# Optimization experiments

Measured on AMD Instinct MI355X. Metric: run time of the kernel, lower is better.

## Reference

```python
import jax, jax.numpy as jnp
import numpy as np

BEV_RANGE = 32.0   # meters; traj xy normalized to [-1,1] by this half-range
NUM_HEADS = 8
EGO_FUT_TS = 8
EPS = 1e-5


def _ln(x, g, b):
    m = x.mean(-1, keepdims=True)
    v = ((x - m) ** 2).mean(-1, keepdims=True)
    return (x - m) / jnp.sqrt(v + EPS) * g + b


def _mha(q, k, v, wq, bq, wk, bk, wv, bv, wo, bo):
    B, Lq, D = q.shape
    Lk = k.shape[1]
    dh = D // NUM_HEADS
    qh = (q @ wq + bq).reshape(B, Lq, NUM_HEADS, dh).transpose(0, 2, 1, 3)
    kh = (k @ wk + bk).reshape(B, Lk, NUM_HEADS, dh).transpose(0, 2, 1, 3)
    vh = (v @ wv + bv).reshape(B, Lk, NUM_HEADS, dh).transpose(0, 2, 1, 3)
    a = jax.nn.softmax(jnp.einsum('bhqd,bhkd->bhqk', qh, kh) * (1.0 / float(np.sqrt(dh))), axis=-1)
    o = jnp.einsum('bhqk,bhkd->bhqd', a, vh).transpose(0, 2, 1, 3).reshape(B, Lq, D)
    return o @ wo + bo


def _grid_sample(value, grid):
    # value (B,C,H,W); grid (B,M,P,2) xy in [-1,1]; bilinear, zeros padding, align_corners=False
    B, C, H, W = value.shape
    x = (grid[..., 0] + 1.0) * (W * 0.5) - 0.5
    y = (grid[..., 1] + 1.0) * (H * 0.5) - 0.5
    x0 = jnp.floor(x)
    y0 = jnp.floor(y)
    bidx = jnp.arange(B)[:, None, None]

    def corner(xi, yi, w):
        valid = (xi >= 0) & (xi <= W - 1) & (yi >= 0) & (yi <= H - 1)
        xc = jnp.clip(xi, 0, W - 1).astype(jnp.int32)
        yc = jnp.clip(yi, 0, H - 1).astype(jnp.int32)
        v = value[bidx, :, yc, xc]  # advanced idx -> (B,M,P,C)
        return v * (w * valid)[..., None]

    return (corner(x0, y0, (x0 + 1 - x) * (y0 + 1 - y))
            + corner(x0 + 1, y0, (x - x0) * (y0 + 1 - y))
            + corner(x0, y0 + 1, (x0 + 1 - x) * (y - y0))
            + corner(x0 + 1, y0 + 1, (x - x0) * (y - y0)))


def _mish(x):
    return x * jnp.tanh(jax.nn.softplus(x))


def _forward(traj_feature, noisy_traj_points, bev_feature, agents_query, ego_query,
             time_embed, status_encoding,
             bev_value_w, bev_value_b, bev_attn_w, bev_attn_b, bev_out_w, bev_out_b,
             aq_wq, aq_bq, aq_wk, aq_bk, aq_wv, aq_bv, aq_wo, aq_bo,
             eq_wq, eq_bq, eq_wk, eq_bk, eq_wv, eq_bv, eq_wo, eq_bo,
             ffn_w1, ffn_b1, ffn_w2, ffn_b2,
             n1_g, n1_b, n2_g, n2_b, n3_g, n3_b,
             mod_w, mod_b,
             cls_w1, cls_b1, cls_ln1_g, cls_ln1_b, cls_w2, cls_b2, cls_ln2_g, cls_ln2_b, cls_w3, cls_b3,
             reg_w1, reg_b1, reg_w2, reg_b2, reg_w3, reg_b3):
    B, M, D = traj_feature.shape
    # --- GridSampleCrossBEVAttention ---
    value = jnp.einsum('bchw,cd->bdhw', bev_feature, bev_value_w) + bev_value_b[None, :, None, None]
    grid = noisy_traj_points / BEV_RANGE                    # (B,M,P,2) in [-1,1]
    sampled = _grid_sample(value, grid)                     # (B,M,P,D)
    pt_w = jax.nn.softmax(traj_feature @ bev_attn_w + bev_attn_b, axis=-1)  # (B,M,P)
    bev_out = jnp.einsum('bmpd,bmp->bmd', sampled, pt_w) @ bev_out_w + bev_out_b
    traj = traj_feature + bev_out
    # --- cross-agent attention + norm1 ---
    traj = _ln(traj + _mha(traj, agents_query, agents_query,
                           aq_wq, aq_bq, aq_wk, aq_bk, aq_wv, aq_bv, aq_wo, aq_bo), n1_g, n1_b)
    # --- cross-ego attention + norm2 ---
    traj = _ln(traj + _mha(traj, ego_query, ego_query,
                           eq_wq, eq_bq, eq_wk, eq_bk, eq_wv, eq_bv, eq_wo, eq_bo), n2_g, n2_b)
    # --- FFN + norm3 (note: no residual, matches source) ---
    traj = _ln(jax.nn.relu(traj @ ffn_w1 + ffn_b1) @ ffn_w2 + ffn_b2, n3_g, n3_b)
    # --- FiLM time modulation ---
    ss = _mish(time_embed) @ mod_w + mod_b                  # (B,1,2D)
    scale, shift = jnp.split(ss, 2, axis=-1)
    traj = traj * (1.0 + scale) + shift
    # --- task decoder: cls branch (linear_relu_ln x2 + Linear->1) ---
    h = _ln(jax.nn.relu(traj @ cls_w1 + cls_b1), cls_ln1_g, cls_ln1_b)
    h = _ln(jax.nn.relu(h @ cls_w2 + cls_b2), cls_ln2_g, cls_ln2_b)
    plan_cls = (h @ cls_w3 + cls_b3)[..., 0]                # (B,M)
    # --- task decoder: reg branch ---
    r = jax.nn.relu(traj @ reg_w1 + reg_b1)
    r = jax.nn.relu(r @ reg_w2 + reg_b2)
    r = (r @ reg_w3 + reg_b3).reshape(B, M, EGO_FUT_TS, 3)
    xy = r[..., :2] + noisy_traj_points
    heading = jnp.tanh(r[..., 2:3]) * np.pi
    poses_reg = jnp.concatenate([xy, heading], axis=-1)     # (B,M,T,3)
    return poses_reg, plan_cls


def setup_inputs() -> dict:
    key = jax.random.key(0)
    ks = iter(jax.random.split(key, 80))
    rn = lambda *s: jax.random.normal(next(ks), s, dtype=jnp.float32)
    w = lambda *s: rn(*s) * 0.05
    B, M, P, D, A, FF = 32, 20, 8, 256, 32, 1024
    inp = dict(
        traj_feature=rn(B, M, D),
        noisy_traj_points=rn(B, M, P, 2) * 8.0,
        bev_feature=rn(B, 256, 128, 128),
        agents_query=rn(B, A, D),
        ego_query=rn(B, 1, D),
        time_embed=rn(B, 1, D),
        status_encoding=rn(B, 1, D),
        bev_value_w=w(256, D), bev_value_b=jnp.zeros(D),
        bev_attn_w=w(D, P), bev_attn_b=jnp.zeros(P),
        bev_out_w=w(D, D), bev_out_b=jnp.zeros(D),
        aq_wq=w(D, D), aq_bq=jnp.zeros(D), aq_wk=w(D, D), aq_bk=jnp.zeros(D),
        aq_wv=w(D, D), aq_bv=jnp.zeros(D), aq_wo=w(D, D), aq_bo=jnp.zeros(D),
        eq_wq=w(D, D), eq_bq=jnp.zeros(D), eq_wk=w(D, D), eq_bk=jnp.zeros(D),
        eq_wv=w(D, D), eq_bv=jnp.zeros(D), eq_wo=w(D, D), eq_bo=jnp.zeros(D),
        ffn_w1=w(D, FF), ffn_b1=jnp.zeros(FF), ffn_w2=w(FF, D), ffn_b2=jnp.zeros(D),
        n1_g=jnp.ones(D), n1_b=jnp.zeros(D), n2_g=jnp.ones(D), n2_b=jnp.zeros(D),
        n3_g=jnp.ones(D), n3_b=jnp.zeros(D),
        mod_w=w(D, 2 * D), mod_b=jnp.zeros(2 * D),
        cls_w1=w(D, D), cls_b1=jnp.zeros(D), cls_ln1_g=jnp.ones(D), cls_ln1_b=jnp.zeros(D),
        cls_w2=w(D, D), cls_b2=jnp.zeros(D), cls_ln2_g=jnp.ones(D), cls_ln2_b=jnp.zeros(D),
        cls_w3=w(D, 1), cls_b3=jnp.full((1,), float(-np.log((1 - 0.01) / 0.01))),
        reg_w1=w(D, D), reg_b1=jnp.zeros(D), reg_w2=w(D, D), reg_b2=jnp.zeros(D),
        reg_w3=w(D, EGO_FUT_TS * 3), reg_b3=jnp.zeros(EGO_FUT_TS * 3),
        bev_spatial_shape=jnp.array([128, 128], dtype=jnp.int32),
    )
    return inp


def reference(traj_feature, noisy_traj_points, bev_feature, agents_query, ego_query,
              time_embed, status_encoding,
              bev_value_w, bev_value_b, bev_attn_w, bev_attn_b, bev_out_w, bev_out_b,
              aq_wq, aq_bq, aq_wk, aq_bk, aq_wv, aq_bv, aq_wo, aq_bo,
              eq_wq, eq_bq, eq_wk, eq_bk, eq_wv, eq_bv, eq_wo, eq_bo,
              ffn_w1, ffn_b1, ffn_w2, ffn_b2,
              n1_g, n1_b, n2_g, n2_b, n3_g, n3_b,
              mod_w, mod_b,
              cls_w1, cls_b1, cls_ln1_g, cls_ln1_b, cls_w2, cls_b2, cls_ln2_g, cls_ln2_b, cls_w3, cls_b3,
              reg_w1, reg_b1, reg_w2, reg_b2, reg_w3, reg_b3,
              bev_spatial_shape):
    # bev_spatial_shape is implied by bev_feature's static shape under jit
    return _forward(traj_feature, noisy_traj_points, bev_feature, agents_query, ego_query,
                    time_embed, status_encoding,
                    bev_value_w, bev_value_b, bev_attn_w, bev_attn_b, bev_out_w, bev_out_b,
                    aq_wq, aq_bq, aq_wk, aq_bk, aq_wv, aq_bv, aq_wo, aq_bo,
                    eq_wq, eq_bq, eq_wk, eq_bk, eq_wv, eq_bv, eq_wo, eq_bo,
                    ffn_w1, ffn_b1, ffn_w2, ffn_b2,
                    n1_g, n1_b, n2_g, n2_b, n3_g, n3_b,
                    mod_w, mod_b,
                    cls_w1, cls_b1, cls_ln1_g, cls_ln1_b, cls_w2, cls_b2, cls_ln2_g, cls_ln2_b, cls_w3, cls_b3,
                    reg_w1, reg_b1, reg_w2, reg_b2, reg_w3, reg_b3)
```

## Files before the change

kernel.cpp:

```cpp
#include <hip/hip_runtime.h>
#include <math.h>

constexpr int NB = 32;
constexpr int NM = 20;
constexpr int NP = 8;
constexpr int ND = 256;
constexpr int NA = 32;
constexpr int NFF = 1024;
constexpr int NH = 128, NW = 128;
constexpr int HW = NH * NW;

constexpr int PK_BVW = 0;
constexpr int PK_BOW = 65536;
constexpr int PK_WQ  = 131072;
constexpr int PK_WO  = 196608;
constexpr int PK_CW1 = 262144;
constexpr int PK_CW2 = 327680;
constexpr int PK_RW1 = 393216;
constexpr int PK_RW2 = 458752;
constexpr int PK_WK  = 524288;
constexpr int PK_WV  = 589824;
constexpr int PK_FW1 = 655360;
constexpr int PK_FW2 = 917504;
constexpr int PK_TOTAL = 1179648;

constexpr int WS_GW   = 0;
constexpr int WS_WSUM = 163840;
constexpr int WS_K1   = 164480;
constexpr int WS_V1   = 426624;
constexpr int WS_U    = 688768;
constexpr int WS_SS   = 696960;
constexpr int WS_PACK = 720896;

__device__ __forceinline__ void dec2(unsigned u, float& f0, float& f1) {
    union { unsigned x; float f; } a, b;
    a.x = u << 16;
    b.x = u & 0xffff0000u;
    f0 = a.f; f1 = b.f;
}

__device__ __forceinline__ float fma4(float4 a, uint2 w, float acc) {
    float w0, w1, w2, w3;
    dec2(w.x, w0, w1);
    dec2(w.y, w2, w3);
    acc += a.x * w0;
    acc += a.y * w1;
    acc += a.z * w2;
    acc += a.w * w3;
    return acc;
}

__device__ __forceinline__ float gemm256(const uint2* __restrict__ wp, const float* __restrict__ sa,
                                         int tid, float acc) {
    const float4* a4 = (const float4*)sa;
    #pragma unroll 8
    for (int c4 = 0; c4 < 64; ++c4) {
        float4 a = a4[c4];
        uint2 w = wp[(c4 << 8) + tid];
        acc = fma4(a, w, acc);
    }
    return acc;
}

struct PackArgs {
    const float* src[12];
    int log2N[12];
    int elems[12];
    int dstoff[12];
};

__global__ void pack_kernel(PackArgs pa, unsigned short* __restrict__ dst) {
    int e = blockIdx.x * 256 + threadIdx.x;
    int seg = 0;
    while (seg < 12 && e >= pa.elems[seg]) { e -= pa.elems[seg]; seg++; }
    if (seg >= 12) return;
    int lg = pa.log2N[seg];
    int N = 1 << lg;
    int c = e >> lg;
    int n = e & (N - 1);
    float v = pa.src[seg][e];
    union { float f; unsigned u; } uu; uu.f = v;
    unsigned x = uu.u;
    unsigned r = (x + 0x7fff + ((x >> 16) & 1)) >> 16;
    int idx = (((c >> 2) << lg) + n) * 4 + (c & 3);
    dst[pa.dstoff[seg] + idx] = (unsigned short)r;
}

__device__ __forceinline__ float blk_sum(float v, float* s_red) {
    for (int off = 32; off > 0; off >>= 1) v += __shfl_down(v, off, 64);
    int tid = threadIdx.x;
    __syncthreads();
    if ((tid & 63) == 0) s_red[tid >> 6] = v;
    __syncthreads();
    return s_red[0] + s_red[1] + s_red[2] + s_red[3];
}

__device__ __forceinline__ float blk_ln(float x, const float* g, const float* bb, float* s_red) {
    int tid = threadIdx.x;
    float mean = blk_sum(x, s_red) * (1.0f / 256.0f);
    float xm = x - mean;
    float var = blk_sum(xm * xm, s_red) * (1.0f / 256.0f);
    return xm / sqrtf(var + 1e-5f) * g[tid] + bb[tid];
}

__global__ void gather_kernel(const float* __restrict__ traj, const float* __restrict__ noisy,
                              const float* __restrict__ bev, const float* __restrict__ attn_w,
                              const float* __restrict__ attn_b,
                              float* __restrict__ gw, float* __restrict__ wsumw) {
    int blk = blockIdx.x;
    int b = blk / NM, tid = threadIdx.x;
    __shared__ float s_traj[ND];
    __shared__ float s_ptw[NP];
    __shared__ float s_w[32];
    __shared__ int s_idx[32];

    s_traj[tid] = traj[(size_t)blk * ND + tid];
    __syncthreads();
    if (tid < NP) {
        float acc = attn_b[tid];
        for (int c = 0; c < ND; c++) acc += s_traj[c] * attn_w[c * NP + tid];
        s_ptw[tid] = acc;
    }
    __syncthreads();
    if (tid == 0) {
        float mx = s_ptw[0];
        for (int p = 1; p < NP; p++) mx = fmaxf(mx, s_ptw[p]);
        float e[NP], sum = 0.f;
        for (int p = 0; p < NP; p++) { e[p] = expf(s_ptw[p] - mx); sum += e[p]; }
        for (int p = 0; p < NP; p++) s_ptw[p] = e[p] / sum;
    }
    __syncthreads();
    if (tid < 32) {
        int p = tid >> 2, corner = tid & 3;
        float gx = noisy[((size_t)blk * NP + p) * 2 + 0] * (1.0f / 32.0f);
        float gy = noisy[((size_t)blk * NP + p) * 2 + 1] * (1.0f / 32.0f);
        float x = (gx + 1.0f) * (NW * 0.5f) - 0.5f;
        float y = (gy + 1.0f) * (NH * 0.5f) - 0.5f;
        float x0 = floorf(x), y0 = floorf(y);
        int dx = corner & 1, dy = corner >> 1;
        float wx = dx ? (x - x0) : (x0 + 1.0f - x);
        float wy = dy ? (y - y0) : (y0 + 1.0f - y);
        float xi = x0 + (float)dx, yi = y0 + (float)dy;
        bool valid = (xi >= 0.f) && (xi <= (float)(NW - 1)) && (yi >= 0.f) && (yi <= (float)(NH - 1));
        int xc = (int)fminf(fmaxf(xi, 0.f), (float)(NW - 1));
        int yc = (int)fminf(fmaxf(yi, 0.f), (float)(NH - 1));
        s_w[tid] = wx * wy * (valid ? 1.f : 0.f) * s_ptw[p];
        s_idx[tid] = yc * NW + xc;
    }
    __syncthreads();
    if (tid == 0) {
        float s = 0.f;
        for (int j = 0; j < 32; j++) s += s_w[j];
        wsumw[blk] = s;
    }
    const float* base = bev + (size_t)b * ND * HW + (size_t)tid * HW;
    float acc0 = 0.f, acc1 = 0.f;
    #pragma unroll
    for (int j = 0; j < 32; j += 2) {
        acc0 += s_w[j]     * base[s_idx[j]];
        acc1 += s_w[j + 1] * base[s_idx[j + 1]];
    }
    gw[(size_t)blk * ND + tid] = acc0 + acc1;
}

__global__ void kv_kernel(const float* __restrict__ agents,
                          const uint2* __restrict__ wkp, const float* __restrict__ bk,
                          const uint2* __restrict__ wvp, const float* __restrict__ bv,
                          float* __restrict__ K1, float* __restrict__ V1) {
    int blk = blockIdx.x, tid = threadIdx.x;
    int a0 = blk * 2;
    __shared__ __align__(16) float s0[ND], s1[ND];
    s0[tid] = agents[(size_t)a0 * ND + tid];
    s1[tid] = agents[(size_t)(a0 + 1) * ND + tid];
    __syncthreads();
    float k0 = bk[tid], k1 = k0, v0 = bv[tid], v1 = v0;
    const float4* p0 = (const float4*)s0;
    const float4* p1 = (const float4*)s1;
    #pragma unroll 8
    for (int c4 = 0; c4 < 64; ++c4) {
        float4 a0f = p0[c4], a1f = p1[c4];
        uint2 wk = wkp[(c4 << 8) + tid];
        uint2 wv = wvp[(c4 << 8) + tid];
        k0 = fma4(a0f, wk, k0); k1 = fma4(a1f, wk, k1);
        v0 = fma4(a0f, wv, v0); v1 = fma4(a1f, wv, v1);
    }
    K1[(size_t)a0 * ND + tid] = k0;
    K1[(size_t)(a0 + 1) * ND + tid] = k1;
    V1[(size_t)a0 * ND + tid] = v0;
    V1[(size_t)(a0 + 1) * ND + tid] = v1;
}

__global__ void perb_kernel(const float* __restrict__ ego,
                            const float* __restrict__ eq_wv, const float* __restrict__ eq_bv,
                            const float* __restrict__ eq_wo, const float* __restrict__ eq_bo,
                            const float* __restrict__ time_embed,
                            const float* __restrict__ mod_w, const float* __restrict__ mod_b,
                            float* __restrict__ u, float* __restrict__ ss) {
    int b = blockIdx.x, tid = threadIdx.x;
    __shared__ float s_a[ND], s_b[ND];
    s_a[tid] = ego[(size_t)b * ND + tid];
    __syncthreads();
    float v = eq_bv[tid];
    for (int c = 0; c < ND; c++) v += s_a[c] * eq_wv[c * ND + tid];
    s_b[tid] = v;
    __syncthreads();
    float o = eq_bo[tid];
    for (int c = 0; c < ND; c++) o += s_b[c] * eq_wo[c * ND + tid];
    u[(size_t)b * ND + tid] = o;

    float te = time_embed[(size_t)b * ND + tid];
    float sp = log1pf(expf(te));
    float me = te * tanhf(sp);
    __syncthreads();
    s_a[tid] = me;
    __syncthreads();
    for (int jj = 0; jj < 2; jj++) {
        int j = tid + jj * ND;
        float acc = mod_b[j];
        for (int c = 0; c < ND; c++) acc += s_a[c] * mod_w[(size_t)c * 2 * ND + j];
        ss[(size_t)b * 2 * ND + j] = acc;
    }
}

struct MegaW {
    const float *traj, *noisy;
    const float *bvb, *bob, *bq, *bo;
    const float *n1g, *n1b, *n2g, *n2b;
    const float *fb1, *fb2, *n3g, *n3b;
    const float *cb1, *cl1g, *cl1b, *cb2, *cl2g, *cl2b, *cw3, *cb3;
    const float *rb1, *rb2, *rw3, *rb3;
};

__global__ void mega_kernel(const float* __restrict__ gw, const float* __restrict__ wsumw,
                            const float* __restrict__ K1, const float* __restrict__ V1,
                            const float* __restrict__ u, const float* __restrict__ ss,
                            const uint2* __restrict__ bvwp, const uint2* __restrict__ bowp,
                            const uint2* __restrict__ wqp, const uint2* __restrict__ wop,
                            const uint2* __restrict__ fw1p, const uint2* __restrict__ fw2p,
                            const uint2* __restrict__ cw1p, const uint2* __restrict__ cw2p,
                            const uint2* __restrict__ rw1p, const uint2* __restrict__ rw2p,
                            MegaW W, float* __restrict__ out) {
    int blk = blockIdx.x;
    int b = blk / NM, tid = threadIdx.x;
    __shared__ __align__(16) float s_a[ND];
    __shared__ __align__(16) float s_b[ND];
    __shared__ __align__(16) float s_h[NFF];
    __shared__ __align__(16) float s_sc[ND];
    __shared__ float s_red[4];

    s_sc[tid] = gw[(size_t)blk * ND + tid];
    float wsw = wsumw[blk];
    __syncthreads();
    float acc = gemm256(bvwp, s_sc, tid, W.bvb[tid] * wsw);
    __syncthreads();
    s_b[tid] = acc;
    __syncthreads();
    acc = gemm256(bowp, s_b, tid, W.bob[tid] + W.traj[(size_t)blk * ND + tid]);
    s_a[tid] = acc;
    __syncthreads();
    acc = gemm256(wqp, s_a, tid, W.bq[tid]);
    __syncthreads();
    s_b[tid] = acc;
    __syncthreads();
    int h = tid >> 5, kk = tid & 31;
    {
        const float* Krow = K1 + ((size_t)(b * NA + kk)) * ND + h * 32;
        float sc = 0.f;
        for (int j = 0; j < 32; j++) sc += s_b[h * 32 + j] * Krow[j];
        s_sc[tid] = sc * 0.17677669529663687f;
    }
    __syncthreads();
    {
        float mx = -1e30f;
        for (int j = 0; j < 32; j++) mx = fmaxf(mx, s_sc[h * 32 + j]);
        float den = 0.f;
        for (int j = 0; j < 32; j++) den += expf(s_sc[h * 32 + j] - mx);
        float p = expf(s_sc[tid] - mx) / den;
        __syncthreads();
        s_sc[tid] = p;
        __syncthreads();
    }
    {
        const float* Vb = V1 + (size_t)b * NA * ND;
        float o = 0.f;
        for (int k = 0; k < 32; k++) o += s_sc[h * 32 + k] * Vb[(size_t)k * ND + tid];
        __syncthreads();
        s_b[tid] = o;
        __syncthreads();
    }
    acc = gemm256(wop, s_b, tid, W.bo[tid] + s_a[tid]);
    float t1 = blk_ln(acc, W.n1g, W.n1b, s_red);
    float t2 = blk_ln(t1 + u[(size_t)b * ND + tid], W.n2g, W.n2b, s_red);
    __syncthreads();
    s_a[tid] = t2;
    __syncthreads();
    {
        float f0 = W.fb1[tid], f1 = W.fb1[tid + 256], f2 = W.fb1[tid + 512], f3 = W.fb1[tid + 768];
        const float4* a4 = (const float4*)s_a;
        #pragma unroll 4
        for (int c4 = 0; c4 < 64; ++c4) {
            float4 a = a4[c4];
            f0 = fma4(a, fw1p[(c4 << 10) + tid], f0);
            f1 = fma4(a, fw1p[(c4 << 10) + 256 + tid], f1);
            f2 = fma4(a, fw1p[(c4 << 10) + 512 + tid], f2);
            f3 = fma4(a, fw1p[(c4 << 10) + 768 + tid], f3);
        }
        s_h[tid] = fmaxf(f0, 0.f);
        s_h[tid + 256] = fmaxf(f1, 0.f);
        s_h[tid + 512] = fmaxf(f2, 0.f);
        s_h[tid + 768] = fmaxf(f3, 0.f);
    }
    __syncthreads();
    {
        acc = W.fb2[tid];
        const float4* h4 = (const float4*)s_h;
        #pragma unroll 8
        for (int c4 = 0; c4 < 256; ++c4) {
            acc = fma4(h4[c4], fw2p[(c4 << 8) + tid], acc);
        }
    }
    float t3 = blk_ln(acc, W.n3g, W.n3b, s_red);
    float sc1 = ss[(size_t)b * 2 * ND + tid];
    float sh1 = ss[(size_t)b * 2 * ND + ND + tid];
    float tt = t3 * (1.f + sc1) + sh1;
    __syncthreads();
    s_a[tid] = tt;
    __syncthreads();
    acc = gemm256(cw1p, s_a, tid, W.cb1[tid]);
    float h1 = blk_ln(fmaxf(acc, 0.f), W.cl1g, W.cl1b, s_red);
    __syncthreads();
    s_b[tid] = h1;
    __syncthreads();
    acc = gemm256(cw2p, s_b, tid, W.cb2[tid]);
    float h2 = blk_ln(fmaxf(acc, 0.f), W.cl2g, W.cl2b, s_red);
    float pc = blk_sum(h2 * W.cw3[tid], s_red);
    if (tid == 0) out[(size_t)NB * NM * NP * 3 + blk] = pc + W.cb3[0];
    acc = gemm256(rw1p, s_a, tid, W.rb1[tid]);
    __syncthreads();
    s_b[tid] = fmaxf(acc, 0.f);
    __syncthreads();
    acc = gemm256(rw2p, s_b, tid, W.rb2[tid]);
    __syncthreads();
    s_b[tid] = fmaxf(acc, 0.f);
    __syncthreads();
    if (tid < 24) {
        float r3 = W.rb3[tid];
        for (int c = 0; c < ND; c++) r3 += s_b[c] * W.rw3[c * 24 + tid];
        int ts = tid / 3, k2 = tid % 3;
        float val;
        if (k2 < 2) val = r3 + W.noisy[((size_t)blk * NP + ts) * 2 + k2];
        else        val = tanhf(r3) * 3.14159265358979323846f;
        out[((size_t)blk * NP + ts) * 3 + k2] = val;
    }
}

extern "C" void kernel_launch(void* const* d_in, const int* in_sizes, int n_in,
                              void* d_out, int out_size, void* d_ws, size_t ws_size,
                              hipStream_t stream) {
    const float* traj   = (const float*)d_in[0];
    const float* noisy  = (const float*)d_in[1];
    const float* bev    = (const float*)d_in[2];
    const float* agents = (const float*)d_in[3];
    const float* ego    = (const float*)d_in[4];
    const float* temb   = (const float*)d_in[5];
    const float* bvw = (const float*)d_in[7];
    const float* bvb = (const float*)d_in[8];
    const float* baw = (const float*)d_in[9];
    const float* bab = (const float*)d_in[10];
    const float* bow = (const float*)d_in[11];
    const float* bob = (const float*)d_in[12];
    const float* aq_wq = (const float*)d_in[13];
    const float* aq_bq = (const float*)d_in[14];
    const float* aq_wk = (const float*)d_in[15];
    const float* aq_bk = (const float*)d_in[16];
    const float* aq_wv = (const float*)d_in[17];
    const float* aq_bv = (const float*)d_in[18];
    const float* aq_wo = (const float*)d_in[19];
    const float* aq_bo = (const float*)d_in[20];
    const float* eq_wv = (const float*)d_in[25];
    const float* eq_bv = (const float*)d_in[26];
    const float* eq_wo = (const float*)d_in[27];
    const float* eq_bo = (const float*)d_in[28];
    const float* fw1 = (const float*)d_in[29];
    const float* fb1 = (const float*)d_in[30];
    const float* fw2 = (const float*)d_in[31];
    const float* fb2 = (const float*)d_in[32];
    const float* n1g = (const float*)d_in[33];
    const float* n1b = (const float*)d_in[34];
    const float* n2g = (const float*)d_in[35];
    const float* n2b = (const float*)d_in[36];
    const float* n3g = (const float*)d_in[37];
    const float* n3b = (const float*)d_in[38];
    const float* modw = (const float*)d_in[39];
    const float* modb = (const float*)d_in[40];
    const float* cw1 = (const float*)d_in[41];
    const float* cb1 = (const float*)d_in[42];
    const float* cl1g = (const float*)d_in[43];
    const float* cl1b = (const float*)d_in[44];
    const float* cw2 = (const float*)d_in[45];
    const float* cb2 = (const float*)d_in[46];
    const float* cl2g = (const float*)d_in[47];
    const float* cl2b = (const float*)d_in[48];
    const float* cw3 = (const float*)d_in[49];
    const float* cb3 = (const float*)d_in[50];
    const float* rw1 = (const float*)d_in[51];
    const float* rb1 = (const float*)d_in[52];
    const float* rw2 = (const float*)d_in[53];
    const float* rb2 = (const float*)d_in[54];
    const float* rw3 = (const float*)d_in[55];
    const float* rb3 = (const float*)d_in[56];

    float* ws = (float*)d_ws;
    float* gw    = ws + WS_GW;
    float* wsumw = ws + WS_WSUM;
    float* K1    = ws + WS_K1;
    float* V1    = ws + WS_V1;
    float* u     = ws + WS_U;
    float* ssb   = ws + WS_SS;
    unsigned short* pk = (unsigned short*)(ws + WS_PACK);

    PackArgs pa;
    const float* srcs[12] = {bvw, bow, aq_wq, aq_wo, cw1, cw2, rw1, rw2, aq_wk, aq_wv, fw1, fw2};
    int lg[12]   = {8, 8, 8, 8, 8, 8, 8, 8, 8, 8, 10, 8};
    int el[12]   = {65536, 65536, 65536, 65536, 65536, 65536, 65536, 65536, 65536, 65536, 262144, 262144};
    int off[12]  = {PK_BVW, PK_BOW, PK_WQ, PK_WO, PK_CW1, PK_CW2, PK_RW1, PK_RW2, PK_WK, PK_WV, PK_FW1, PK_FW2};
    for (int i = 0; i < 12; i++) { pa.src[i] = srcs[i]; pa.log2N[i] = lg[i]; pa.elems[i] = el[i]; pa.dstoff[i] = off[i]; }
    pack_kernel<<<dim3(PK_TOTAL / 256), dim3(256), 0, stream>>>(pa, pk);

    gather_kernel<<<dim3(NB * NM), dim3(256), 0, stream>>>(traj, noisy, bev, baw, bab, gw, wsumw);
    kv_kernel<<<dim3(NB * NA / 2), dim3(256), 0, stream>>>(agents,
        (const uint2*)(pk + PK_WK), aq_bk, (const uint2*)(pk + PK_WV), aq_bv, K1, V1);
    perb_kernel<<<dim3(NB), dim3(256), 0, stream>>>(ego, eq_wv, eq_bv, eq_wo, eq_bo, temb, modw, modb, u, ssb);

    MegaW W;
    W.traj = traj; W.noisy = noisy;
    W.bvb = bvb; W.bob = bob; W.bq = aq_bq; W.bo = aq_bo;
    W.n1g = n1g; W.n1b = n1b; W.n2g = n2g; W.n2b = n2b;
    W.fb1 = fb1; W.fb2 = fb2; W.n3g = n3g; W.n3b = n3b;
    W.cb1 = cb1; W.cl1g = cl1g; W.cl1b = cl1b;
    W.cb2 = cb2; W.cl2g = cl2g; W.cl2b = cl2b; W.cw3 = cw3; W.cb3 = cb3;
    W.rb1 = rb1; W.rb2 = rb2; W.rw3 = rw3; W.rb3 = rb3;

    mega_kernel<<<dim3(NB * NM), dim3(256), 0, stream>>>(gw, wsumw, K1, V1, u, ssb,
        (const uint2*)(pk + PK_BVW), (const uint2*)(pk + PK_BOW),
        (const uint2*)(pk + PK_WQ),  (const uint2*)(pk + PK_WO),
        (const uint2*)(pk + PK_FW1), (const uint2*)(pk + PK_FW2),
        (const uint2*)(pk + PK_CW1), (const uint2*)(pk + PK_CW2),
        (const uint2*)(pk + PK_RW1), (const uint2*)(pk + PK_RW2),
        W, (float*)d_out);
}
```

Baseline: 890.9 us.

## Fuse prologue kernels into one launch and process two tokens per mega block

Merges the pack, gather, K/V projection and per-batch kernels into a single prologue kernel, dispatching on block index. The K/V projection now reads fp32 weights directly, four agents per block, so those weights no longer need packing first. The mega kernel runs 512-thread blocks that each handle two tokens, with reductions split per half-block. The aim is to cut launch and dependency overhead and reuse weight loads across two tokens, at the cost of more shared memory per block and occupancy limits set through launch bounds.

```diff
diff --git a/kernel.cpp b/kernel.cpp
--- a/kernel.cpp
+++ b/kernel.cpp
@@ -18,11 +18,9 @@
 constexpr int PK_CW2 = 327680;
 constexpr int PK_RW1 = 393216;
 constexpr int PK_RW2 = 458752;
-constexpr int PK_WK  = 524288;
-constexpr int PK_WV  = 589824;
 constexpr int PK_FW1 = 655360;
 constexpr int PK_FW2 = 917504;
-constexpr int PK_TOTAL = 1179648;
+constexpr int PK_ELEMS = 1048576;
 
 constexpr int WS_GW   = 0;
 constexpr int WS_WSUM = 163840;
@@ -51,175 +49,181 @@
 }
 
 __device__ __forceinline__ float gemm256(const uint2* __restrict__ wp, const float* __restrict__ sa,
-                                         int tid, float acc) {
+                                         int t, float acc) {
     const float4* a4 = (const float4*)sa;
     #pragma unroll 8
     for (int c4 = 0; c4 < 64; ++c4) {
         float4 a = a4[c4];
-        uint2 w = wp[(c4 << 8) + tid];
+        uint2 w = wp[(c4 << 8) + t];
         acc = fma4(a, w, acc);
     }
     return acc;
 }
 
+constexpr int GB_GATHER = NB * NM;
+constexpr int GB_KV     = NB * NA / 4;
+constexpr int GB_PERB   = NB;
+constexpr int GB_PACK   = PK_ELEMS / 256;
+constexpr int PRO_GRID  = GB_GATHER + GB_KV + GB_PERB + GB_PACK;
+
 struct PackArgs {
-    const float* src[12];
-    int log2N[12];
-    int elems[12];
-    int dstoff[12];
+    const float* src[10];
+    int log2N[10];
+    int elems[10];
+    int dstoff[10];
 };
 
-__global__ void pack_kernel(PackArgs pa, unsigned short* __restrict__ dst) {
-    int e = blockIdx.x * 256 + threadIdx.x;
-    int seg = 0;
-    while (seg < 12 && e >= pa.elems[seg]) { e -= pa.elems[seg]; seg++; }
-    if (seg >= 12) return;
-    int lg = pa.log2N[seg];
-    int N = 1 << lg;
-    int c = e >> lg;
-    int n = e & (N - 1);
-    float v = pa.src[seg][e];
-    union { float f; unsigned u; } uu; uu.f = v;
-    unsigned x = uu.u;
-    unsigned r = (x + 0x7fff + ((x >> 16) & 1)) >> 16;
-    int idx = (((c >> 2) << lg) + n) * 4 + (c & 3);
-    dst[pa.dstoff[seg] + idx] = (unsigned short)r;
-}
-
-__device__ __forceinline__ float blk_sum(float v, float* s_red) {
-    for (int off = 32; off > 0; off >>= 1) v += __shfl_down(v, off, 64);
-    int tid = threadIdx.x;
-    __syncthreads();
-    if ((tid & 63) == 0) s_red[tid >> 6] = v;
-    __syncthreads();
-    return s_red[0] + s_red[1] + s_red[2] + s_red[3];
-}
-
-__device__ __forceinline__ float blk_ln(float x, const float* g, const float* bb, float* s_red) {
-    int tid = threadIdx.x;
-    float mean = blk_sum(x, s_red) * (1.0f / 256.0f);
-    float xm = x - mean;
-    float var = blk_sum(xm * xm, s_red) * (1.0f / 256.0f);
-    return xm / sqrtf(var + 1e-5f) * g[tid] + bb[tid];
-}
-
-__global__ void gather_kernel(const float* __restrict__ traj, const float* __restrict__ noisy,
-                              const float* __restrict__ bev, const float* __restrict__ attn_w,
-                              const float* __restrict__ attn_b,
-                              float* __restrict__ gw, float* __restrict__ wsumw) {
-    int blk = blockIdx.x;
-    int b = blk / NM, tid = threadIdx.x;
-    __shared__ float s_traj[ND];
+struct ProArgs {
+    const float *traj, *noisy, *bev, *attn_w, *attn_b;
+    const float *agents, *wk, *bk, *wv, *bv;
+    const float *ego, *eq_wv, *eq_bv, *eq_wo, *eq_bo;
+    const float *temb, *modw, *modb;
+    float *gw, *wsum, *K1, *V1, *u, *ss;
+    unsigned short* pk;
+};
+
+__global__ void prologue_kernel(ProArgs A, PackArgs pa) {
+    int blk = blockIdx.x, tid = threadIdx.x;
+    __shared__ __align__(16) float sm0[ND];
+    __shared__ __align__(16) float sm1[ND];
+    __shared__ __align__(16) float sm2[ND];
+    __shared__ __align__(16) float sm3[ND];
     __shared__ float s_ptw[NP];
     __shared__ float s_w[32];
     __shared__ int s_idx[32];
 
-    s_traj[tid] = traj[(size_t)blk * ND + tid];
-    __syncthreads();
-    if (tid < NP) {
-        float acc = attn_b[tid];
-        for (int c = 0; c < ND; c++) acc += s_traj[c] * attn_w[c * NP + tid];
-        s_ptw[tid] = acc;
-    }
-    __syncthreads();
-    if (tid == 0) {
-        float mx = s_ptw[0];
-        for (int p = 1; p < NP; p++) mx = fmaxf(mx, s_ptw[p]);
-        float e[NP], sum = 0.f;
-        for (int p = 0; p < NP; p++) { e[p] = expf(s_ptw[p] - mx); sum += e[p]; }
-        for (int p = 0; p < NP; p++) s_ptw[p] = e[p] / sum;
-    }
-    __syncthreads();
-    if (tid < 32) {
-        int p = tid >> 2, corner = tid & 3;
-        float gx = noisy[((size_t)blk * NP + p) * 2 + 0] * (1.0f / 32.0f);
-        float gy = noisy[((size_t)blk * NP + p) * 2 + 1] * (1.0f / 32.0f);
-        float x = (gx + 1.0f) * (NW * 0.5f) - 0.5f;
-        float y = (gy + 1.0f) * (NH * 0.5f) - 0.5f;
-        float x0 = floorf(x), y0 = floorf(y);
-        int dx = corner & 1, dy = corner >> 1;
-        float wx = dx ? (x - x0) : (x0 + 1.0f - x);
-        float wy = dy ? (y - y0) : (y0 + 1.0f - y);
-        float xi = x0 + (float)dx, yi = y0 + (float)dy;
-        bool valid = (xi >= 0.f) && (xi <= (float)(NW - 1)) && (yi >= 0.f) && (yi <= (float)(NH - 1));
-        int xc = (int)fminf(fmaxf(xi, 0.f), (float)(NW - 1));
-        int yc = (int)fminf(fmaxf(yi, 0.f), (float)(NH - 1));
-        s_w[tid] = wx * wy * (valid ? 1.f : 0.f) * s_ptw[p];
-        s_idx[tid] = yc * NW + xc;
-    }
-    __syncthreads();
-    if (tid == 0) {
-        float s = 0.f;
-        for (int j = 0; j < 32; j++) s += s_w[j];
-        wsumw[blk] = s;
-    }
-    const float* base = bev + (size_t)b * ND * HW + (size_t)tid * HW;
-    float acc0 = 0.f, acc1 = 0.f;
-    #pragma unroll
-    for (int j = 0; j < 32; j += 2) {
-        acc0 += s_w[j]     * base[s_idx[j]];
-        acc1 += s_w[j + 1] * base[s_idx[j + 1]];
-    }
-    gw[(size_t)blk * ND + tid] = acc0 + acc1;
-}
-
-__global__ void kv_kernel(const float* __restrict__ agents,
-                          const uint2* __restrict__ wkp, const float* __restrict__ bk,
-                          const uint2* __restrict__ wvp, const float* __restrict__ bv,
-                          float* __restrict__ K1, float* __restrict__ V1) {
-    int blk = blockIdx.x, tid = threadIdx.x;
-    int a0 = blk * 2;
-    __shared__ __align__(16) float s0[ND], s1[ND];
-    s0[tid] = agents[(size_t)a0 * ND + tid];
-    s1[tid] = agents[(size_t)(a0 + 1) * ND + tid];
-    __syncthreads();
-    float k0 = bk[tid], k1 = k0, v0 = bv[tid], v1 = v0;
-    const float4* p0 = (const float4*)s0;
-    const float4* p1 = (const float4*)s1;
-    #pragma unroll 8
-    for (int c4 = 0; c4 < 64; ++c4) {
-        float4 a0f = p0[c4], a1f = p1[c4];
-        uint2 wk = wkp[(c4 << 8) + tid];
-        uint2 wv = wvp[(c4 << 8) + tid];
-        k0 = fma4(a0f, wk, k0); k1 = fma4(a1f, wk, k1);
-        v0 = fma4(a0f, wv, v0); v1 = fma4(a1f, wv, v1);
-    }
-    K1[(size_t)a0 * ND + tid] = k0;
-    K1[(size_t)(a0 + 1) * ND + tid] = k1;
-    V1[(size_t)a0 * ND + tid] = v0;
-    V1[(size_t)(a0 + 1) * ND + tid] = v1;
-}
-
-__global__ void perb_kernel(const float* __restrict__ ego,
-                            const float* __restrict__ eq_wv, const float* __restrict__ eq_bv,
-                            const float* __restrict__ eq_wo, const float* __restrict__ eq_bo,
-                            const float* __restrict__ time_embed,
-                            const float* __restrict__ mod_w, const float* __restrict__ mod_b,
-                            float* __restrict__ u, float* __restrict__ ss) {
-    int b = blockIdx.x, tid = threadIdx.x;
-    __shared__ float s_a[ND], s_b[ND];
-    s_a[tid] = ego[(size_t)b * ND + tid];
-    __syncthreads();
-    float v = eq_bv[tid];
-    for (int c = 0; c < ND; c++) v += s_a[c] * eq_wv[c * ND + tid];
-    s_b[tid] = v;
-    __syncthreads();
-    float o = eq_bo[tid];
-    for (int c = 0; c < ND; c++) o += s_b[c] * eq_wo[c * ND + tid];
-    u[(size_t)b * ND + tid] = o;
-
-    float te = time_embed[(size_t)b * ND + tid];
-    float sp = log1pf(expf(te));
-    float me = te * tanhf(sp);
-    __syncthreads();
-    s_a[tid] = me;
-    __syncthreads();
-    for (int jj = 0; jj < 2; jj++) {
-        int j = tid + jj * ND;
-        float acc = mod_b[j];
-        for (int c = 0; c < ND; c++) acc += s_a[c] * mod_w[(size_t)c * 2 * ND + j];
-        ss[(size_t)b * 2 * ND + j] = acc;
-    }
+    if (blk < GB_GATHER) {
+        int b = blk / NM;
+        sm0[tid] = A.traj[(size_t)blk * ND + tid];
+        __syncthreads();
+        if (tid < NP) {
+            float acc = A.attn_b[tid];
+            for (int c = 0; c < ND; c++) acc += sm0[c] * A.attn_w[c * NP + tid];
+            s_ptw[tid] = acc;
+        }
+        __syncthreads();
+        if (tid == 0) {
+            float mx = s_ptw[0];
+            for (int p = 1; p < NP; p++) mx = fmaxf(mx, s_ptw[p]);
+            float e[NP], sum = 0.f;
+            for (int p = 0; p < NP; p++) { e[p] = expf(s_ptw[p] - mx); sum += e[p]; }
+            for (int p = 0; p < NP; p++) s_ptw[p] = e[p] / sum;
+        }
+        __syncthreads();
+        if (tid < 32) {
+            int p = tid >> 2, corner = tid & 3;
+            float gx = A.noisy[((size_t)blk * NP + p) * 2 + 0] * (1.0f / 32.0f);
+            float gy = A.noisy[((size_t)blk * NP + p) * 2 + 1] * (1.0f / 32.0f);
+            float x = (gx + 1.0f) * (NW * 0.5f) - 0.5f;
+            float y = (gy + 1.0f) * (NH * 0.5f) - 0.5f;
+            float x0 = floorf(x), y0 = floorf(y);
+            int dx = corner & 1, dy = corner >> 1;
+            float wx = dx ? (x - x0) : (x0 + 1.0f - x);
+            float wy = dy ? (y - y0) : (y0 + 1.0f - y);
+            float xi = x0 + (float)dx, yi = y0 + (float)dy;
+            bool valid = (xi >= 0.f) && (xi <= (float)(NW - 1)) && (yi >= 0.f) && (yi <= (float)(NH - 1));
+            int xc = (int)fminf(fmaxf(xi, 0.f), (float)(NW - 1));
+            int yc = (int)fminf(fmaxf(yi, 0.f), (float)(NH - 1));
+            s_w[tid] = wx * wy * (valid ? 1.f : 0.f) * s_ptw[p];
+            s_idx[tid] = yc * NW + xc;
+        }
+        __syncthreads();
+        if (tid == 0) {
+            float s = 0.f;
+            for (int j = 0; j < 32; j++) s += s_w[j];
+            A.wsum[blk] = s;
+        }
+        const float* base = A.bev + (size_t)b * ND * HW + (size_t)tid * HW;
+        float acc0 = 0.f, acc1 = 0.f;
+        #pragma unroll
+        for (int j = 0; j < 32; j += 2) {
+            acc0 += s_w[j]     * base[s_idx[j]];
+            acc1 += s_w[j + 1] * base[s_idx[j + 1]];
+        }
+        A.gw[(size_t)blk * ND + tid] = acc0 + acc1;
+    } else if (blk < GB_GATHER + GB_KV) {
+        int a0 = (blk - GB_GATHER) * 4;
+        sm0[tid] = A.agents[(size_t)a0 * ND + tid];
+        sm1[tid] = A.agents[(size_t)(a0 + 1) * ND + tid];
+        sm2[tid] = A.agents[(size_t)(a0 + 2) * ND + tid];
+        sm3[tid] = A.agents[(size_t)(a0 + 3) * ND + tid];
+        __syncthreads();
+        float k0 = A.bk[tid], k1 = k0, k2 = k0, k3 = k0;
+        float v0 = A.bv[tid], v1 = v0, v2 = v0, v3 = v0;
+        #pragma unroll 4
+        for (int c = 0; c < ND; ++c) {
+            float wk = A.wk[(size_t)c * ND + tid];
+            float wv = A.wv[(size_t)c * ND + tid];
+            float a0f = sm0[c], a1f = sm1[c], a2f = sm2[c], a3f = sm3[c];
+            k0 += a0f * wk; k1 += a1f * wk; k2 += a2f * wk; k3 += a3f * wk;
+            v0 += a0f * wv; v1 += a1f * wv; v2 += a2f * wv; v3 += a3f * wv;
+        }
+        A.K1[(size_t)a0 * ND + tid] = k0;
+        A.K1[(size_t)(a0 + 1) * ND + tid] = k1;
+        A.K1[(size_t)(a0 + 2) * ND + tid] = k2;
+        A.K1[(size_t)(a0 + 3) * ND + tid] = k3;
+        A.V1[(size_t)a0 * ND + tid] = v0;
+        A.V1[(size_t)(a0 + 1) * ND + tid] = v1;
+        A.V1[(size_t)(a0 + 2) * ND + tid] = v2;
+        A.V1[(size_t)(a0 + 3) * ND + tid] = v3;
+    } else if (blk < GB_GATHER + GB_KV + GB_PERB) {
+        int b = blk - (GB_GATHER + GB_KV);
+        sm0[tid] = A.ego[(size_t)b * ND + tid];
+        __syncthreads();
+        float v = A.eq_bv[tid];
+        for (int c = 0; c < ND; c++) v += sm0[c] * A.eq_wv[c * ND + tid];
+        sm1[tid] = v;
+        __syncthreads();
+        float o = A.eq_bo[tid];
+        for (int c = 0; c < ND; c++) o += sm1[c] * A.eq_wo[c * ND + tid];
+        A.u[(size_t)b * ND + tid] = o;
+
+        float te = A.temb[(size_t)b * ND + tid];
+        float sp = log1pf(expf(te));
+        float me = te * tanhf(sp);
+        __syncthreads();
+        sm0[tid] = me;
+        __syncthreads();
+        for (int jj = 0; jj < 2; jj++) {
+            int j = tid + jj * ND;
+            float acc = A.modb[j];
+            for (int c = 0; c < ND; c++) acc += sm0[c] * A.modw[(size_t)c * 2 * ND + j];
+            A.ss[(size_t)b * 2 * ND + j] = acc;
+        }
+    } else {
+        int e = (blk - (GB_GATHER + GB_KV + GB_PERB)) * 256 + tid;
+        int seg = 0;
+        while (seg < 10 && e >= pa.elems[seg]) { e -= pa.elems[seg]; seg++; }
+        if (seg < 10) {
+            int lg = pa.log2N[seg];
+            int N = 1 << lg;
+            int c = e >> lg;
+            int n = e & (N - 1);
+            float v = pa.src[seg][e];
+            union { float f; unsigned u; } uu; uu.f = v;
+            unsigned x = uu.u;
+            unsigned r = (x + 0x7fff + ((x >> 16) & 1)) >> 16;
+            int idx = (((c >> 2) << lg) + n) * 4 + (c & 3);
+            A.pk[pa.dstoff[seg] + idx] = (unsigned short)r;
+        }
+    }
+}
+
+__device__ __forceinline__ float half_sum(float v, float* s_red, int tid) {
+    for (int off = 32; off > 0; off >>= 1) v += __shfl_down(v, off, 64);
+    __syncthreads();
+    if ((tid & 63) == 0) s_red[tid >> 6] = v;
+    __syncthreads();
+    int base = (tid >> 8) << 2;
+    return s_red[base] + s_red[base + 1] + s_red[base + 2] + s_red[base + 3];
+}
+
+__device__ __forceinline__ float half_ln(float x, const float* g, const float* bb, float* s_red, int tid) {
+    int t = tid & 255;
+    float mean = half_sum(x, s_red, tid) * (1.0f / 256.0f);
+    float xm = x - mean;
+    float var = half_sum(xm * xm, s_red, tid) * (1.0f / 256.0f);
+    return xm / sqrtf(var + 1e-5f) * g[t] + bb[t];
 }
 
 struct MegaW {
@@ -231,126 +235,131 @@
     const float *rb1, *rb2, *rw3, *rb3;
 };
 
-__global__ void mega_kernel(const float* __restrict__ gw, const float* __restrict__ wsumw,
-                            const float* __restrict__ K1, const float* __restrict__ V1,
-                            const float* __restrict__ u, const float* __restrict__ ss,
-                            const uint2* __restrict__ bvwp, const uint2* __restrict__ bowp,
-                            const uint2* __restrict__ wqp, const uint2* __restrict__ wop,
-                            const uint2* __restrict__ fw1p, const uint2* __restrict__ fw2p,
-                            const uint2* __restrict__ cw1p, const uint2* __restrict__ cw2p,
-                            const uint2* __restrict__ rw1p, const uint2* __restrict__ rw2p,
-                            MegaW W, float* __restrict__ out) {
+__global__ __launch_bounds__(512, 4)
+void mega_kernel(const float* __restrict__ gw, const float* __restrict__ wsumw,
+                 const float* __restrict__ K1, const float* __restrict__ V1,
+                 const float* __restrict__ u, const float* __restrict__ ss,
+                 const uint2* __restrict__ bvwp, const uint2* __restrict__ bowp,
+                 const uint2* __restrict__ wqp, const uint2* __restrict__ wop,
+                 const uint2* __restrict__ fw1p, const uint2* __restrict__ fw2p,
+                 const uint2* __restrict__ cw1p, const uint2* __restrict__ cw2p,
+                 const uint2* __restrict__ rw1p, const uint2* __restrict__ rw2p,
+                 MegaW W, float* __restrict__ out) {
     int blk = blockIdx.x;
-    int b = blk / NM, tid = threadIdx.x;
-    __shared__ __align__(16) float s_a[ND];
-    __shared__ __align__(16) float s_b[ND];
-    __shared__ __align__(16) float s_h[NFF];
-    __shared__ __align__(16) float s_sc[ND];
-    __shared__ float s_red[4];
-
-    s_sc[tid] = gw[(size_t)blk * ND + tid];
-    float wsw = wsumw[blk];
-    __syncthreads();
-    float acc = gemm256(bvwp, s_sc, tid, W.bvb[tid] * wsw);
-    __syncthreads();
-    s_b[tid] = acc;
-    __syncthreads();
-    acc = gemm256(bowp, s_b, tid, W.bob[tid] + W.traj[(size_t)blk * ND + tid]);
-    s_a[tid] = acc;
-    __syncthreads();
-    acc = gemm256(wqp, s_a, tid, W.bq[tid]);
-    __syncthreads();
-    s_b[tid] = acc;
-    __syncthreads();
-    int h = tid >> 5, kk = tid & 31;
+    int tid = threadIdx.x;
+    int half = tid >> 8;
+    int t = tid & 255;
+    int tok = blk * 2 + half;
+    int b = tok / NM;
+    __shared__ __align__(16) float s_a[2][ND];
+    __shared__ __align__(16) float s_b[2][ND];
+    __shared__ __align__(16) float s_h[2][NFF];
+    __shared__ __align__(16) float s_sc[2][ND];
+    __shared__ float s_red[8];
+
+    s_sc[half][t] = gw[(size_t)tok * ND + t];
+    float wsw = wsumw[tok];
+    __syncthreads();
+    float acc = gemm256(bvwp, s_sc[half], t, W.bvb[t] * wsw);
+    __syncthreads();
+    s_b[half][t] = acc;
+    __syncthreads();
+    acc = gemm256(bowp, s_b[half], t, W.bob[t] + W.traj[(size_t)tok * ND + t]);
+    s_a[half][t] = acc;
+    __syncthreads();
+    acc = gemm256(wqp, s_a[half], t, W.bq[t]);
+    __syncthreads();
+    s_b[half][t] = acc;
+    __syncthreads();
+    int h = t >> 5, kk = t & 31;
     {
         const float* Krow = K1 + ((size_t)(b * NA + kk)) * ND + h * 32;
         float sc = 0.f;
-        for (int j = 0; j < 32; j++) sc += s_b[h * 32 + j] * Krow[j];
-        s_sc[tid] = sc * 0.17677669529663687f;
+        for (int j = 0; j < 32; j++) sc += s_b[half][h * 32 + j] * Krow[j];
+        s_sc[half][t] = sc * 0.17677669529663687f;
     }
     __syncthreads();
     {
         float mx = -1e30f;
-        for (int j = 0; j < 32; j++) mx = fmaxf(mx, s_sc[h * 32 + j]);
+        for (int j = 0; j < 32; j++) mx = fmaxf(mx, s_sc[half][h * 32 + j]);
         float den = 0.f;
-        for (int j = 0; j < 32; j++) den += expf(s_sc[h * 32 + j] - mx);
-        float p = expf(s_sc[tid] - mx) / den;
-        __syncthreads();
-        s_sc[tid] = p;
+        for (int j = 0; j < 32; j++) den += expf(s_sc[half][h * 32 + j] - mx);
+        float p = expf(s_sc[half][t] - mx) / den;
+        __syncthreads();
+        s_sc[half][t] = p;
         __syncthreads();
     }
     {
         const float* Vb = V1 + (size_t)b * NA * ND;
         float o = 0.f;
-        for (int k = 0; k < 32; k++) o += s_sc[h * 32 + k] * Vb[(size_t)k * ND + tid];
-        __syncthreads();
-        s_b[tid] = o;
-        __syncthreads();
-    }
-    acc = gemm256(wop, s_b, tid, W.bo[tid] + s_a[tid]);
-    float t1 = blk_ln(acc, W.n1g, W.n1b, s_red);
-    float t2 = blk_ln(t1 + u[(size_t)b * ND + tid], W.n2g, W.n2b, s_red);
-    __syncthreads();
-    s_a[tid] = t2;
+        for (int k = 0; k < 32; k++) o += s_sc[half][h * 32 + k] * Vb[(size_t)k * ND + t];
+        __syncthreads();
+        s_b[half][t] = o;
+        __syncthreads();
+    }
+    acc = gemm256(wop, s_b[half], t, W.bo[t] + s_a[half][t]);
+    float t1 = half_ln(acc, W.n1g, W.n1b, s_red, tid);
+    float t2 = half_ln(t1 + u[(size_t)b * ND + t], W.n2g, W.n2b, s_red, tid);
+    __syncthreads();
+    s_a[half][t] = t2;
     __syncthreads();
     {
-        float f0 = W.fb1[tid], f1 = W.fb1[tid + 256], f2 = W.fb1[tid + 512], f3 = W.fb1[tid + 768];
-        const float4* a4 = (const float4*)s_a;
+        float f0 = W.fb1[t], f1 = W.fb1[t + 256], f2 = W.fb1[t + 512], f3 = W.fb1[t + 768];
+        const float4* a4 = (const float4*)s_a[half];
         #pragma unroll 4
         for (int c4 = 0; c4 < 64; ++c4) {
             float4 a = a4[c4];
-            f0 = fma4(a, fw1p[(c4 << 10) + tid], f0);
-            f1 = fma4(a, fw1p[(c4 << 10) + 256 + tid], f1);
-            f2 = fma4(a, fw1p[(c4 << 10) + 512 + tid], f2);
-            f3 = fma4(a, fw1p[(c4 << 10) + 768 + tid], f3);
-        }
-        s_h[tid] = fmaxf(f0, 0.f);
-        s_h[tid + 256] = fmaxf(f1, 0.f);
-        s_h[tid + 512] = fmaxf(f2, 0.f);
-        s_h[tid + 768] = fmaxf(f3, 0.f);
+            f0 = fma4(a, fw1p[(c4 << 10) + t], f0);
+            f1 = fma4(a, fw1p[(c4 << 10) + 256 + t], f1);
+            f2 = fma4(a, fw1p[(c4 << 10) + 512 + t], f2);
+            f3 = fma4(a, fw1p[(c4 << 10) + 768 + t], f3);
+        }
+        s_h[half][t] = fmaxf(f0, 0.f);
+        s_h[half][t + 256] = fmaxf(f1, 0.f);
+        s_h[half][t + 512] = fmaxf(f2, 0.f);
+        s_h[half][t + 768] = fmaxf(f3, 0.f);
     }
     __syncthreads();
     {
-        acc = W.fb2[tid];
-        const float4* h4 = (const float4*)s_h;
+        acc = W.fb2[t];
+        const float4* h4 = (const float4*)s_h[half];
         #pragma unroll 8
         for (int c4 = 0; c4 < 256; ++c4) {
-            acc = fma4(h4[c4], fw2p[(c4 << 8) + tid], acc);
-        }
-    }
-    float t3 = blk_ln(acc, W.n3g, W.n3b, s_red);
-    float sc1 = ss[(size_t)b * 2 * ND + tid];
-    float sh1 = ss[(size_t)b * 2 * ND + ND + tid];
+            acc = fma4(h4[c4], fw2p[(c4 << 8) + t], acc);
+        }
+    }
+    float t3 = half_ln(acc, W.n3g, W.n3b, s_red, tid);
+    float sc1 = ss[(size_t)b * 2 * ND + t];
+    float sh1 = ss[(size_t)b * 2 * ND + ND + t];
     float tt = t3 * (1.f + sc1) + sh1;
     __syncthreads();
-    s_a[tid] = tt;
-    __syncthreads();
-    acc = gemm256(cw1p, s_a, tid, W.cb1[tid]);
-    float h1 = blk_ln(fmaxf(acc, 0.f), W.cl1g, W.cl1b, s_red);
-    __syncthreads();
-    s_b[tid] = h1;
-    __syncthreads();
-    acc = gemm256(cw2p, s_b, tid, W.cb2[tid]);
-    float h2 = blk_ln(fmaxf(acc, 0.f), W.cl2g, W.cl2b, s_red);
-    float pc = blk_sum(h2 * W.cw3[tid], s_red);
-    if (tid == 0) out[(size_t)NB * NM * NP * 3 + blk] = pc + W.cb3[0];
-    acc = gemm256(rw1p, s_a, tid, W.rb1[tid]);
-    __syncthreads();
-    s_b[tid] = fmaxf(acc, 0.f);
-    __syncthreads();
-    acc = gemm256(rw2p, s_b, tid, W.rb2[tid]);
-    __syncthreads();
-    s_b[tid] = fmaxf(acc, 0.f);
-    __syncthreads();
-    if (tid < 24) {
-        float r3 = W.rb3[tid];
-        for (int c = 0; c < ND; c++) r3 += s_b[c] * W.rw3[c * 24 + tid];
-        int ts = tid / 3, k2 = tid % 3;
+    s_a[half][t] = tt;
+    __syncthreads();
+    acc = gemm256(cw1p, s_a[half], t, W.cb1[t]);
+    float h1 = half_ln(fmaxf(acc, 0.f), W.cl1g, W.cl1b, s_red, tid);
+    __syncthreads();
+    s_b[half][t] = h1;
+    __syncthreads();
+    acc = gemm256(cw2p, s_b[half], t, W.cb2[t]);
+    float h2 = half_ln(fmaxf(acc, 0.f), W.cl2g, W.cl2b, s_red, tid);
+    float pc = half_sum(h2 * W.cw3[t], s_red, tid);
+    if (t == 0) out[(size_t)NB * NM * NP * 3 + tok] = pc + W.cb3[0];
+    acc = gemm256(rw1p, s_a[half], t, W.rb1[t]);
+    __syncthreads();
+    s_b[half][t] = fmaxf(acc, 0.f);
+    __syncthreads();
+    acc = gemm256(rw2p, s_b[half], t, W.rb2[t]);
+    __syncthreads();
+    s_b[half][t] = fmaxf(acc, 0.f);
+    __syncthreads();
+    if (t < 24) {
+        float r3 = W.rb3[t];
+        for (int c = 0; c < ND; c++) r3 += s_b[half][c] * W.rw3[c * 24 + t];
+        int ts = t / 3, k2 = t % 3;
         float val;
-        if (k2 < 2) val = r3 + W.noisy[((size_t)blk * NP + ts) * 2 + k2];
+        if (k2 < 2) val = r3 + W.noisy[((size_t)tok * NP + ts) * 2 + k2];
         else        val = tanhf(r3) * 3.14159265358979323846f;
-        out[((size_t)blk * NP + ts) * 3 + k2] = val;
+        out[((size_t)tok * NP + ts) * 3 + k2] = val;
     }
 }
 
@@ -420,17 +429,21 @@
     unsigned short* pk = (unsigned short*)(ws + WS_PACK);
 
     PackArgs pa;
-    const float* srcs[12] = {bvw, bow, aq_wq, aq_wo, cw1, cw2, rw1, rw2, aq_wk, aq_wv, fw1, fw2};
-    int lg[12]   = {8, 8, 8, 8, 8, 8, 8, 8, 8, 8, 10, 8};
-    int el[12]   = {65536, 65536, 65536, 65536, 65536, 65536, 65536, 65536, 65536, 65536, 262144, 262144};
-    int off[12]  = {PK_BVW, PK_BOW, PK_WQ, PK_WO, PK_CW1, PK_CW2, PK_RW1, PK_RW2, PK_WK, PK_WV, PK_FW1, PK_FW2};
-    for (int i = 0; i < 12; i++) { pa.src[i] = srcs[i]; pa.log2N[i] = lg[i]; pa.elems[i] = el[i]; pa.dstoff[i] = off[i]; }
-    pack_kernel<<<dim3(PK_TOTAL / 256), dim3(256), 0, stream>>>(pa, pk);
-
-    gather_kernel<<<dim3(NB * NM), dim3(256), 0, stream>>>(traj, noisy, bev, baw, bab, gw, wsumw);
-    kv_kernel<<<dim3(NB * NA / 2), dim3(256), 0, stream>>>(agents,
-        (const uint2*)(pk + PK_WK), aq_bk, (const uint2*)(pk + PK_WV), aq_bv, K1, V1);
-    perb_kernel<<<dim3(NB), dim3(256), 0, stream>>>(ego, eq_wv, eq_bv, eq_wo, eq_bo, temb, modw, modb, u, ssb);
+    const float* srcs[10] = {bvw, bow, aq_wq, aq_wo, cw1, cw2, rw1, rw2, fw1, fw2};
+    int lg[10]  = {8, 8, 8, 8, 8, 8, 8, 8, 10, 8};
+    int el[10]  = {65536, 65536, 65536, 65536, 65536, 65536, 65536, 65536, 262144, 262144};
+    int off[10] = {PK_BVW, PK_BOW, PK_WQ, PK_WO, PK_CW1, PK_CW2, PK_RW1, PK_RW2, PK_FW1, PK_FW2};
+    for (int i = 0; i < 10; i++) { pa.src[i] = srcs[i]; pa.log2N[i] = lg[i]; pa.elems[i] = el[i]; pa.dstoff[i] = off[i]; }
+
+    ProArgs PA;
+    PA.traj = traj; PA.noisy = noisy; PA.bev = bev; PA.attn_w = baw; PA.attn_b = bab;
+    PA.agents = agents; PA.wk = aq_wk; PA.bk = aq_bk; PA.wv = aq_wv; PA.bv = aq_bv;
+    PA.ego = ego; PA.eq_wv = eq_wv; PA.eq_bv = eq_bv; PA.eq_wo = eq_wo; PA.eq_bo = eq_bo;
+    PA.temb = temb; PA.modw = modw; PA.modb = modb;
+    PA.gw = gw; PA.wsum = wsumw; PA.K1 = K1; PA.V1 = V1; PA.u = u; PA.ss = ssb;
+    PA.pk = pk;
+
+    prologue_kernel<<<dim3(PRO_GRID), dim3(256), 0, stream>>>(PA, pa);
 
     MegaW W;
     W.traj = traj; W.noisy = noisy;
@@ -441,7 +454,7 @@
     W.cb2 = cb2; W.cl2g = cl2g; W.cl2b = cl2b; W.cw3 = cw3; W.cb3 = cb3;
     W.rb1 = rb1; W.rb2 = rb2; W.rw3 = rw3; W.rb3 = rb3;
 
-    mega_kernel<<<dim3(NB * NM), dim3(256), 0, stream>>>(gw, wsumw, K1, V1, u, ssb,
+    mega_kernel<<<dim3(NB * NM / 2), dim3(512), 0, stream>>>(gw, wsumw, K1, V1, u, ssb,
         (const uint2*)(pk + PK_BVW), (const uint2*)(pk + PK_BOW),
         (const uint2*)(pk + PK_WQ),  (const uint2*)(pk + PK_WO),
         (const uint2*)(pk + PK_FW1), (const uint2*)(pk + PK_FW2),
```

New measurement: 875.3 us. Within noise of the previous version (-1.7%).
